# Kernel tuning notes

Hardware: AMD Instinct MI355X
Metric: run time of the kernel (lower is better)

## Reference

```python
import jax, jax.numpy as jnp
import numpy as np

N_USERS, N_ITEMS, EMB_DIM, N_INTENTS, N_EDGES, N_LAYERS = 50000, 100000, 64, 128, 3000000, 2
N_NODES = N_USERS + N_ITEMS


def _l2norm(x, eps=1e-8):
    # F.normalize(p=2, dim=-1, eps): x / max(||x||, eps)
    n = jnp.sqrt(jnp.sum(x * x, axis=-1, keepdims=True))
    return x / jnp.maximum(n, eps)


def setup_inputs() -> dict:
    key = jax.random.key(0)
    k0, k1, k2, k3, k4, k5 = jax.random.split(key, 6)
    xav_e = np.sqrt(2.0 / (N_NODES + EMB_DIM)).astype(np.float32)
    xav_i = np.sqrt(2.0 / (EMB_DIM + N_INTENTS)).astype(np.float32)
    return {
        "user_emb": jax.random.normal(k0, (N_USERS, EMB_DIM), jnp.float32) * xav_e,
        "item_emb": jax.random.normal(k1, (N_ITEMS, EMB_DIM), jnp.float32) * xav_e,
        "user_intent": jax.random.normal(k2, (EMB_DIM, N_INTENTS), jnp.float32) * xav_i,
        "item_intent": jax.random.normal(k3, (EMB_DIM, N_INTENTS), jnp.float32) * xav_i,
        "all_h": jax.random.randint(k4, (N_EDGES,), 0, N_NODES, jnp.int32),
        "all_t": jax.random.randint(k5, (N_EDGES,), 0, N_NODES, jnp.int32),
    }


def reference(user_emb, item_emb, user_intent, item_intent, all_h, all_t):
    E = all_h.shape[0]

    def spmm(vals, x):
        # y[h] += vals * x[t]  over edges  (torch_sparse.spmm)
        return jax.ops.segment_sum(vals[:, None] * x[all_t], all_h, num_segments=N_NODES)

    # _cal_sparse_adj: G = D^-1/2 A D^-1/2 on the unweighted edge list
    deg = jax.ops.segment_sum(jnp.ones((E,), jnp.float32), all_h, num_segments=N_NODES)
    d_inv_sqrt = jnp.where(deg > 0, deg, 1.0) ** -0.5 * (deg > 0)
    g_values = d_inv_sqrt[all_h] * d_inv_sqrt[all_t]

    def adaptive_values(src):
        # _adaptive_mask: cosine-sim edge weights, row-normalized
        he = _l2norm(src[all_h])
        te = _l2norm(src[all_t])
        edge_alpha = (jnp.sum(he * te, axis=1) + 1.0) * 0.5  # in [0,1]
        row_sum = jax.ops.segment_sum(edge_alpha, all_h, num_segments=N_NODES)
        d_inv = jnp.where(row_sum > 0, 1.0 / jnp.where(row_sum > 0, row_sum, 1.0), 0.0)
        return d_inv[all_h] * edge_alpha

    emb = jnp.concatenate([user_emb, item_emb], axis=0)  # [N, d]
    acc = emb
    for _ in range(N_LAYERS):
        gnn = spmm(g_values, emb)
        u, it = emb[:N_USERS], emb[N_USERS:]
        u_int = jax.nn.softmax(u @ user_intent, axis=1) @ user_intent.T
        i_int = jax.nn.softmax(it @ item_intent, axis=1) @ item_intent.T
        int_e = jnp.concatenate([u_int, i_int], axis=0)
        gaa = spmm(adaptive_values(gnn), emb)
        iaa = spmm(adaptive_values(int_e), emb)
        emb = gnn + int_e + gaa + iaa + emb
        acc = acc + emb
    # torch: sum over stacked layer embeddings == initial + each layer output
    return acc
```

## Files before the change

### kernel.cpp

```cpp
#include <hip/hip_runtime.h>
#include <hip/hip_bf16.h>

#define N_USERS   50000
#define N_ITEMS   100000
#define N_NODES   150000
#define DIM       64
#define N_INTENTS 128
#define N_EDGES   3000000
#define PSHIFT    9
#define PROWS     (1 << PSHIFT)
#define NPART     ((N_NODES + PROWS - 1) >> PSHIFT)
#define CHUNK     16384
#define NCHB      ((N_EDGES + CHUNK - 1) / CHUNK)

typedef __attribute__((ext_vector_type(8))) short short8v;
typedef __attribute__((ext_vector_type(4))) float f32x4;

static __device__ __forceinline__ float wsum64(float v){
#pragma unroll
  for (int m = 32; m >= 1; m >>= 1) v += __shfl_xor(v, m, 64);
  return v;
}

template<int CTRL>
static __device__ __forceinline__ float dpp_ror_add(float x){
  int t = __builtin_amdgcn_update_dpp(0, __builtin_bit_cast(int, x),
                                      CTRL, 0xF, 0xF, true);
  return x + __builtin_bit_cast(float, t);
}
static __device__ __forceinline__ float row16_allsum(float x){
  x = dpp_ror_add<0x128>(x);
  x = dpp_ror_add<0x124>(x);
  x = dpp_ror_add<0x122>(x);
  x = dpp_ror_add<0x121>(x);
  return x;
}
template<int CTRL>
static __device__ __forceinline__ float dpp_ror_max(float x){
  int t = __builtin_amdgcn_update_dpp(0, __builtin_bit_cast(int, x),
                                      CTRL, 0xF, 0xF, true);
  return fmaxf(x, __builtin_bit_cast(float, t));
}
static __device__ __forceinline__ float row16_allmax(float x){
  x = dpp_ror_max<0x128>(x);
  x = dpp_ror_max<0x124>(x);
  x = dpp_ror_max<0x122>(x);
  x = dpp_ror_max<0x121>(x);
  return x;
}

static __device__ __forceinline__ unsigned short f2bf(float x){
  __hip_bfloat16 h = __float2bfloat16(x);
  return __builtin_bit_cast(unsigned short, h);
}
static __device__ __forceinline__ float bf_lo(unsigned int v){
  return __builtin_bit_cast(float, v << 16);
}
static __device__ __forceinline__ float bf_hi(unsigned int v){
  return __builtin_bit_cast(float, v & 0xFFFF0000u);
}
static __device__ __forceinline__ float bfval(unsigned short h){
  return __builtin_bit_cast(float, (unsigned int)h << 16);
}
static __device__ __forceinline__ void split2(float x, unsigned short& hi,
                                              unsigned short& lo){
  hi = f2bf(x);
  lo = f2bf(x - bfval(hi));
}

__global__ void k_init(const float* __restrict__ ue, const float* __restrict__ ie,
                       float* __restrict__ emb, float* __restrict__ acc,
                       unsigned short* __restrict__ embb){
  int i = blockIdx.x * 256 + threadIdx.x;
  if (i >= N_NODES * DIM) return;
  float v = (i < N_USERS * DIM) ? ue[i] : ie[i - N_USERS * DIM];
  emb[i] = v; acc[i] = v; embb[i] = f2bf(v);
}

__global__ void k_deg(const int* __restrict__ h, int* __restrict__ deg){
  int e = blockIdx.x * 256 + threadIdx.x;
  if (e < N_EDGES) atomicAdd(&deg[h[e]], 1);
}

__global__ void k_scan1(const int* __restrict__ deg, int* __restrict__ tmp,
                        int* __restrict__ aux){
  __shared__ int s[256];
  int t = threadIdx.x, i = blockIdx.x * 256 + t;
  int v = (i < N_NODES) ? deg[i] : 0;
  s[t] = v; __syncthreads();
  for (int off = 1; off < 256; off <<= 1){
    int x = (t >= off) ? s[t - off] : 0;
    __syncthreads();
    s[t] += x;
    __syncthreads();
  }
  if (i < N_NODES) tmp[i] = s[t];
  if (t == 255) aux[blockIdx.x] = s[255];
}

__global__ __launch_bounds__(1024) void k_scan2(int* __restrict__ aux, int n){
  __shared__ int s[1024];
  int t = threadIdx.x;
  int v = (t < n) ? aux[t] : 0;
  s[t] = v; __syncthreads();
  for (int off = 1; off < 1024; off <<= 1){
    int x = (t >= off) ? s[t - off] : 0;
    __syncthreads();
    s[t] += x;
    __syncthreads();
  }
  if (t < n) aux[t] = s[t] - v;
}

__global__ void k_rowptr(const int* __restrict__ tmp, const int* __restrict__ deg,
                         const int* __restrict__ aux, int* __restrict__ rp,
                         float* __restrict__ dis, int* __restrict__ gcur){
  int i = blockIdx.x * 256 + threadIdx.x;
  if (i < N_NODES){
    int v = aux[i >> 8] + tmp[i] - deg[i];
    rp[i] = v;
    int d = deg[i];
    dis[i] = (d > 0) ? (1.f / sqrtf((float)d)) : 0.f;
    if ((i & (PROWS - 1)) == 0) gcur[i >> PSHIFT] = v;
  }
  if (i == 0) rp[N_NODES] = N_EDGES;
}

__global__ __launch_bounds__(256) void k_part1(const int* __restrict__ h,
                                               const int* __restrict__ t,
                                               int* __restrict__ gcur,
                                               unsigned int* __restrict__ stg){
  __shared__ int hist[NPART];
  __shared__ int base[NPART];
  __shared__ int cnt2[NPART];
  int tid = threadIdx.x;
  int s = blockIdx.x * CHUNK;
  int e = min(s + CHUNK, N_EDGES);
  for (int p = tid; p < NPART; p += 256){ hist[p] = 0; cnt2[p] = 0; }
  __syncthreads();
  for (int i = s + tid; i < e; i += 256)
    atomicAdd(&hist[h[i] >> PSHIFT], 1);
  __syncthreads();
  for (int p = tid; p < NPART; p += 256){
    int c = hist[p];
    base[p] = c ? atomicAdd(&gcur[p], c) : 0;
  }
  __syncthreads();
  for (int i = s + tid; i < e; i += 256){
    int hh = h[i];
    int part = hh >> PSHIFT;
    int pos = base[part] + atomicAdd(&cnt2[part], 1);
    stg[pos] = ((unsigned)t[i] << PSHIFT) | (unsigned)(hh & (PROWS - 1));
  }
}

__global__ __launch_bounds__(256) void k_part2(const int* __restrict__ rp,
                                               const unsigned int* __restrict__ stg,
                                               int* __restrict__ t_csr){
  __shared__ int cur[PROWS];
  int b = blockIdx.x, tid = threadIdx.x;
  int row0 = b << PSHIFT;
  int rows = min(PROWS, N_NODES - row0);
  for (int i = tid; i < rows; i += 256) cur[i] = rp[row0 + i];
  __syncthreads();
  int s = rp[row0], e = rp[row0 + rows];
  for (int i = s + tid; i < e; i += 256){
    unsigned int v = stg[i];
    int pos = atomicAdd(&cur[v & (PROWS - 1)], 1);
    t_csr[pos] = (int)(v >> PSHIFT);
  }
}

__global__ void k_spmm_gnn(const int* __restrict__ rp, const int* __restrict__ t_csr,
                           const float* __restrict__ dis,
                           const unsigned short* __restrict__ embb,
                           float* __restrict__ gnn, unsigned short* __restrict__ hgAB){
  int w = (blockIdx.x * 256 + threadIdx.x) >> 6;
  int lane = threadIdx.x & 63;
  if (w >= N_NODES) return;
  int slot = lane >> 3, sub = lane & 7;
  int s = rp[w], e = rp[w + 1];
  float a0=0.f,a1=0.f,a2=0.f,a3=0.f,a4=0.f,a5=0.f,a6=0.f,a7=0.f;
  for (int i = s + slot; i < e; i += 8){
    int t = t_csr[i];
    float wt = dis[t];
    uint4 ev = *(const uint4*)(embb + (size_t)t * 64 + 8 * sub);
    a0 = fmaf(wt, bf_lo(ev.x), a0); a1 = fmaf(wt, bf_hi(ev.x), a1);
    a2 = fmaf(wt, bf_lo(ev.y), a2); a3 = fmaf(wt, bf_hi(ev.y), a3);
    a4 = fmaf(wt, bf_lo(ev.z), a4); a5 = fmaf(wt, bf_hi(ev.z), a5);
    a6 = fmaf(wt, bf_lo(ev.w), a6); a7 = fmaf(wt, bf_hi(ev.w), a7);
  }
#pragma unroll
  for (int m = 8; m <= 32; m <<= 1){
    a0 += __shfl_xor(a0, m, 64); a1 += __shfl_xor(a1, m, 64);
    a2 += __shfl_xor(a2, m, 64); a3 += __shfl_xor(a3, m, 64);
    a4 += __shfl_xor(a4, m, 64); a5 += __shfl_xor(a5, m, 64);
    a6 += __shfl_xor(a6, m, 64); a7 += __shfl_xor(a7, m, 64);
  }
  float dw = dis[w];
  float g0 = dw*a0, g1 = dw*a1, g2 = dw*a2, g3 = dw*a3;
  float g4 = dw*a4, g5 = dw*a5, g6 = dw*a6, g7 = dw*a7;
  float sq = g0*g0 + g1*g1 + g2*g2 + g3*g3 + g4*g4 + g5*g5 + g6*g6 + g7*g7;
#pragma unroll
  for (int m = 1; m <= 4; m <<= 1) sq += __shfl_xor(sq, m, 64);
  float invn = 1.f / fmaxf(sqrtf(sq), 1e-8f);
  if (slot == 0){
    float4 v0 = make_float4(g0, g1, g2, g3);
    float4 v1 = make_float4(g4, g5, g6, g7);
    ((float4*)gnn)[w * 16 + 2 * sub]     = v0;
    ((float4*)gnn)[w * 16 + 2 * sub + 1] = v1;
    uint4 ob;
    ob.x = (unsigned)f2bf(g0*invn) | ((unsigned)f2bf(g1*invn) << 16);
    ob.y = (unsigned)f2bf(g2*invn) | ((unsigned)f2bf(g3*invn) << 16);
    ob.z = (unsigned)f2bf(g4*invn) | ((unsigned)f2bf(g5*invn) << 16);
    ob.w = (unsigned)f2bf(g6*invn) | ((unsigned)f2bf(g7*invn) << 16);
    *(uint4*)(hgAB + (size_t)w * 128 + 8 * sub) = ob;
  }
}

__global__ void k_wprep(const float* __restrict__ wu, const float* __restrict__ wi,
                        unsigned short* __restrict__ wbuf){
  const float* W = blockIdx.x ? wi : wu;
  unsigned short* seg = wbuf + blockIdx.x * 32768;
  int tid = threadIdx.x;
  for (int i = tid; i < DIM * N_INTENTS; i += 256){
    unsigned short h, l; split2(W[i], h, l);
    seg[16384 + i] = h; seg[24576 + i] = l;
  }
  for (int idx = tid; idx < 16 * 64; idx += 256){
    int f = idx >> 6, lane = idx & 63;
    int nt = f >> 1, ks = f & 1, g = lane >> 4, c = lane & 15;
    int in = 16 * nt + c;
#pragma unroll
    for (int e = 0; e < 8; e++){
      int d = 8 * g + e + 32 * ks;
      unsigned short h, l; split2(W[d * N_INTENTS + in], h, l);
      seg[f * 512 + lane * 8 + e] = h;
      seg[8192 + f * 512 + lane * 8 + e] = l;
    }
  }
}

__global__ __launch_bounds__(256) void k_intent_mfma(
    const unsigned short* __restrict__ wseg, const float* __restrict__ emb,
    unsigned short* __restrict__ out_bf, unsigned short* __restrict__ hgAB,
    int base_node, int count){
  __shared__ __align__(16) unsigned int Pl[4][2048];
  int wid = threadIdx.x >> 6, lane = threadIdx.x & 63;
  int tile = blockIdx.x * 4 + wid;
  if (tile * 16 >= count) return;
  int g = lane >> 4, c = lane & 15;

  const float4* erow = (const float4*)(emb + (size_t)(base_node + tile * 16 + c) * DIM);
  float4 ea0 = erow[2 * g],     eb0 = erow[2 * g + 1];
  float4 ea1 = erow[8 + 2 * g], eb1 = erow[9 + 2 * g];
  short8v ehi[2], elo[2];
  {
    float xs[16] = {ea0.x, ea0.y, ea0.z, ea0.w, eb0.x, eb0.y, eb0.z, eb0.w,
                    ea1.x, ea1.y, ea1.z, ea1.w, eb1.x, eb1.y, eb1.z, eb1.w};
#pragma unroll
    for (int ksi = 0; ksi < 2; ksi++)
#pragma unroll
      for (int e = 0; e < 8; e++){
        unsigned short h, l; split2(xs[ksi * 8 + e], h, l);
        ehi[ksi][e] = (short)h; elo[ksi][e] = (short)l;
      }
  }

  const uint4* w1hi = (const uint4*)wseg;
  const uint4* w1lo = (const uint4*)(wseg + 8192);
  f32x4 acc1[8];
#pragma unroll
  for (int nt = 0; nt < 8; nt++){
    f32x4 a = {0.f, 0.f, 0.f, 0.f};
#pragma unroll
    for (int ks = 0; ks < 2; ks++){
      short8v wh = __builtin_bit_cast(short8v, w1hi[(nt * 2 + ks) * 64 + lane]);
      short8v wl = __builtin_bit_cast(short8v, w1lo[(nt * 2 + ks) * 64 + lane]);
      a = __builtin_amdgcn_mfma_f32_16x16x32_bf16(ehi[ks], wh, a, 0, 0, 0);
      a = __builtin_amdgcn_mfma_f32_16x16x32_bf16(elo[ks], wh, a, 0, 0, 0);
      a = __builtin_amdgcn_mfma_f32_16x16x32_bf16(ehi[ks], wl, a, 0, 0, 0);
    }
    acc1[nt] = a;
  }

  unsigned int* pw = &Pl[wid][0];
#pragma unroll
  for (int r = 0; r < 4; r++){
    float m = acc1[0][r];
#pragma unroll
    for (int nt = 1; nt < 8; nt++) m = fmaxf(m, acc1[nt][r]);
    m = row16_allmax(m);
    float p[8];
    float s = 0.f;
#pragma unroll
    for (int nt = 0; nt < 8; nt++){ p[nt] = __expf(acc1[nt][r] - m); s += p[nt]; }
    s = row16_allsum(s);
    float inv = 1.f / s;
    int node = 4 * g + r;
    int swz = (node & 7) << 2;
    int base = node * 128 + c;
#pragma unroll
    for (int nt = 0; nt < 8; nt++){
      float v = p[nt] * inv;
      unsigned short h, l; split2(v, h, l);
      pw[(base + 16 * nt) ^ swz] = (unsigned int)h | ((unsigned int)l << 16);
    }
  }

  const uint4* pr = (const uint4*)pw;
  short8v phf[4], plf[4];
  int sw = (c & 7) << 2;
#pragma unroll
  for (int ks = 0; ks < 4; ks++){
    int i0 = c * 128 + 8 * g + 32 * ks;
    uint4 ra = pr[(i0 ^ sw) >> 2];
    uint4 rb = pr[((i0 + 4) ^ sw) >> 2];
    unsigned int q[8] = {ra.x, ra.y, ra.z, ra.w, rb.x, rb.y, rb.z, rb.w};
#pragma unroll
    for (int e = 0; e < 8; e++){
      phf[ks][e] = (short)(q[e] & 0xFFFFu);
      plf[ks][e] = (short)(q[e] >> 16);
    }
  }

  const uint4* w2hi = (const uint4*)(wseg + 16384);
  const uint4* w2lo = (const uint4*)(wseg + 24576);
  f32x4 acc2[4];
#pragma unroll
  for (int nt = 0; nt < 4; nt++){
    f32x4 a = {0.f, 0.f, 0.f, 0.f};
#pragma unroll
    for (int ks = 0; ks < 4; ks++){
      int fi = (16 * nt + c) * 16 + ks * 4 + g;
      short8v wh = __builtin_bit_cast(short8v, w2hi[fi]);
      short8v wl = __builtin_bit_cast(short8v, w2lo[fi]);
      a = __builtin_amdgcn_mfma_f32_16x16x32_bf16(phf[ks], wh, a, 0, 0, 0);
      a = __builtin_amdgcn_mfma_f32_16x16x32_bf16(plf[ks], wh, a, 0, 0, 0);
      a = __builtin_amdgcn_mfma_f32_16x16x32_bf16(phf[ks], wl, a, 0, 0, 0);
    }
    acc2[nt] = a;
  }

#pragma unroll
  for (int r = 0; r < 4; r++){
    float sq = 0.f;
#pragma unroll
    for (int nt = 0; nt < 4; nt++) sq = fmaf(acc2[nt][r], acc2[nt][r], sq);
    sq = row16_allsum(sq);
    float invn = 1.f / fmaxf(sqrtf(sq), 1e-8f);
    size_t node = (size_t)(base_node + tile * 16 + 4 * g + r);
    unsigned short* hw = hgAB + node * 128 + 64;
    size_t obase = node * DIM + c;
#pragma unroll
    for (int nt = 0; nt < 4; nt++){
      float v = acc2[nt][r];
      out_bf[obase + 16 * nt] = f2bf(v);
      hw[16 * nt + c] = f2bf(v * invn);
    }
  }
}

__global__ void k_adafuse(const int* __restrict__ rp, const int* __restrict__ t_csr,
                          const uint4* __restrict__ hgAB4,
                          const uint2* __restrict__ inte_bf2,
                          const uint2* __restrict__ embb2,
                          const float* __restrict__ emb,
                          float* __restrict__ gnn_io, float* __restrict__ acc,
                          uint2* __restrict__ embb_next2){
  int w = (blockIdx.x * 256 + threadIdx.x) >> 6;
  int lane = threadIdx.x & 63;
  if (w >= N_NODES) return;
  int slot = lane >> 4, sub = lane & 15;
  uint4 hp = hgAB4[(size_t)w * 16 + sub];
  float w0 = bf_lo(hp.x), w1 = bf_hi(hp.x), w2 = bf_lo(hp.y), w3 = bf_hi(hp.y);
  float w4 = bf_lo(hp.z), w5 = bf_hi(hp.z), w6 = bf_lo(hp.w), w7 = bf_hi(hp.w);
  bool isA = sub < 8;
  int s = rp[w], e = rp[w + 1];
  float4 s1 = make_float4(0.f, 0.f, 0.f, 0.f);
  float4 s2 = make_float4(0.f, 0.f, 0.f, 0.f);
  float r1 = 0.f, r2 = 0.f;
  for (int i = s + slot; i < e; i += 4){
    int t = t_csr[i];
    uint4 tp = hgAB4[(size_t)t * 16 + sub];
    float part = w0 * bf_lo(tp.x) + w1 * bf_hi(tp.x)
               + w2 * bf_lo(tp.y) + w3 * bf_hi(tp.y)
               + w4 * bf_lo(tp.z) + w5 * bf_hi(tp.z)
               + w6 * bf_lo(tp.w) + w7 * bf_hi(tp.w);
    float p = row16_allsum(isA ? part : 0.f);
    float q = row16_allsum(isA ? 0.f : part);
    float a1 = fmaf(p, 0.5f, 0.5f);
    float a2 = fmaf(q, 0.5f, 0.5f);
    r1 += a1; r2 += a2;
    uint2 ev = embb2[(size_t)t * 16 + sub];
    float v0 = bf_lo(ev.x), v1 = bf_hi(ev.x), v2 = bf_lo(ev.y), v3 = bf_hi(ev.y);
    s1.x = fmaf(a1, v0, s1.x); s1.y = fmaf(a1, v1, s1.y);
    s1.z = fmaf(a1, v2, s1.z); s1.w = fmaf(a1, v3, s1.w);
    s2.x = fmaf(a2, v0, s2.x); s2.y = fmaf(a2, v1, s2.y);
    s2.z = fmaf(a2, v2, s2.z); s2.w = fmaf(a2, v3, s2.w);
  }
#pragma unroll
  for (int m = 16; m <= 32; m <<= 1){
    s1.x += __shfl_xor(s1.x, m, 64); s1.y += __shfl_xor(s1.y, m, 64);
    s1.z += __shfl_xor(s1.z, m, 64); s1.w += __shfl_xor(s1.w, m, 64);
    s2.x += __shfl_xor(s2.x, m, 64); s2.y += __shfl_xor(s2.y, m, 64);
    s2.z += __shfl_xor(s2.z, m, 64); s2.w += __shfl_xor(s2.w, m, 64);
    r1   += __shfl_xor(r1,   m, 64); r2   += __shfl_xor(r2,   m, 64);
  }
  float d1 = (r1 > 0.f) ? 1.f / r1 : 0.f;
  float d2 = (r2 > 0.f) ? 1.f / r2 : 0.f;
  if (slot == 0){
    int idx4 = w * 16 + sub;
    float4 gg = ((float4*)gnn_io)[idx4];
    uint2 it = inte_bf2[idx4];
    float4 em = ((const float4*)emb)[idx4];
    float4 nv;
    nv.x = gg.x + bf_lo(it.x) + em.x + d1 * s1.x + d2 * s2.x;
    nv.y = gg.y + bf_hi(it.x) + em.y + d1 * s1.y + d2 * s2.y;
    nv.z = gg.z + bf_lo(it.y) + em.z + d1 * s1.z + d2 * s2.z;
    nv.w = gg.w + bf_hi(it.y) + em.w + d1 * s1.w + d2 * s2.w;
    ((float4*)gnn_io)[idx4] = nv;
    float4 ac = ((float4*)acc)[idx4];
    ac.x += nv.x; ac.y += nv.y; ac.z += nv.z; ac.w += nv.w;
    ((float4*)acc)[idx4] = ac;
    uint2 ob;
    ob.x = (unsigned)f2bf(nv.x) | ((unsigned)f2bf(nv.y) << 16);
    ob.y = (unsigned)f2bf(nv.z) | ((unsigned)f2bf(nv.w) << 16);
    embb_next2[idx4] = ob;
  }
}

extern "C" void kernel_launch(void* const* d_in, const int* in_sizes, int n_in,
                              void* d_out, int out_size, void* d_ws, size_t ws_size,
                              hipStream_t stream){
  const float* ue = (const float*)d_in[0];
  const float* ie = (const float*)d_in[1];
  const float* wu = (const float*)d_in[2];
  const float* wi = (const float*)d_in[3];
  const int* all_h = (const int*)d_in[4];
  const int* all_t = (const int*)d_in[5];
  float* acc = (float*)d_out;

  char* p = (char*)d_ws;
  auto take = [&](size_t bytes)->char*{
    char* r = p; p += (bytes + 255) & ~size_t(255); return r;
  };
  float*  embA  = (float*)take(sizeof(float) * N_NODES * DIM);
  float*  embB  = (float*)take(sizeof(float) * N_NODES * DIM);
  unsigned short* hgAB = (unsigned short*)take(sizeof(short) * N_NODES * 128);
  unsigned short* inte_bf = (unsigned short*)take(sizeof(short) * N_NODES * DIM);
  unsigned short* embbA   = (unsigned short*)take(sizeof(short) * N_NODES * DIM);
  unsigned short* embbB   = (unsigned short*)take(sizeof(short) * N_NODES * DIM);
  unsigned short* wbuf    = (unsigned short*)take(sizeof(short) * 2 * 32768);
  int*    t_csr = (int*)take(sizeof(int) * N_EDGES);
  float*  dis   = (float*)take(sizeof(float) * N_NODES);
  int*    deg   = (int*)take(sizeof(int) * N_NODES);
  int*    tmp   = (int*)take(sizeof(int) * N_NODES);
  int*    aux   = (int*)take(sizeof(int) * 1024);
  int*    rp    = (int*)take(sizeof(int) * (N_NODES + 1));
  int*    gcur  = (int*)take(sizeof(int) * NPART);
  if ((size_t)(p - (char*)d_ws) > ws_size) return;
  unsigned int* stg = (unsigned int*)hgAB;

  const int ELEM_B  = (N_NODES * DIM + 255) / 256;
  const int NODEW_B = (N_NODES * 64 + 255) / 256;
  const int EDGE_B  = (N_EDGES + 255) / 256;
  const int NODE_B  = (N_NODES + 255) / 256;

  hipMemsetAsync(deg, 0, sizeof(int) * N_NODES, stream);
  k_init<<<ELEM_B, 256, 0, stream>>>(ue, ie, embA, acc, embbA);
  k_wprep<<<2, 256, 0, stream>>>(wu, wi, wbuf);
  k_deg<<<EDGE_B, 256, 0, stream>>>(all_h, deg);
  k_scan1<<<NODE_B, 256, 0, stream>>>(deg, tmp, aux);
  k_scan2<<<1, 1024, 0, stream>>>(aux, NODE_B);
  k_rowptr<<<NODE_B, 256, 0, stream>>>(tmp, deg, aux, rp, dis, gcur);
  k_part1<<<NCHB, 256, 0, stream>>>(all_h, all_t, gcur, stg);
  k_part2<<<NPART, 256, 0, stream>>>(rp, stg, t_csr);

  const int UT_B = ((N_USERS / 16) + 3) / 4;
  const int IT_B = ((N_ITEMS / 16) + 3) / 4;

  float* eA = embA;
  float* eB = embB;
  unsigned short* ebA = embbA;
  unsigned short* ebB = embbB;
  for (int layer = 0; layer < 2; layer++){
    k_spmm_gnn<<<NODEW_B, 256, 0, stream>>>(rp, t_csr, dis, ebA, eB, hgAB);
    k_intent_mfma<<<UT_B, 256, 0, stream>>>(wbuf, eA, inte_bf, hgAB, 0, N_USERS);
    k_intent_mfma<<<IT_B, 256, 0, stream>>>(wbuf + 32768, eA, inte_bf, hgAB,
                                            N_USERS, N_ITEMS);
    k_adafuse<<<NODEW_B, 256, 0, stream>>>(rp, t_csr, (const uint4*)hgAB,
                                           (const uint2*)inte_bf,
                                           (const uint2*)ebA,
                                           eA, eB, acc, (uint2*)ebB);
    float* t = eA; eA = eB; eB = t;
    unsigned short* tb = ebA; ebA = ebB; ebB = tb;
  }
}
```

Measured before the change: 1.008 ms.

## Store normalized edge-similarity embeddings in FP8 and pre-scale gathered embeddings by degree

```diff
diff --git a/kernel.cpp b/kernel.cpp
--- a/kernel.cpp
+++ b/kernel.cpp
@@ -15,12 +15,7 @@
 
 typedef __attribute__((ext_vector_type(8))) short short8v;
 typedef __attribute__((ext_vector_type(4))) float f32x4;
-
-static __device__ __forceinline__ float wsum64(float v){
-#pragma unroll
-  for (int m = 32; m >= 1; m >>= 1) v += __shfl_xor(v, m, 64);
-  return v;
-}
+typedef __attribute__((ext_vector_type(2))) float f32x2;
 
 template<int CTRL>
 static __device__ __forceinline__ float dpp_ror_add(float x){
@@ -66,6 +61,18 @@
                                               unsigned short& lo){
   hi = f2bf(x);
   lo = f2bf(x - bfval(hi));
+}
+
+static __device__ __forceinline__ void fp8dec8(uint2 v, float* f){
+  f32x2 a = __builtin_amdgcn_cvt_pk_f32_fp8(v.x, false);
+  f32x2 b = __builtin_amdgcn_cvt_pk_f32_fp8(v.x, true);
+  f32x2 c = __builtin_amdgcn_cvt_pk_f32_fp8(v.y, false);
+  f32x2 d = __builtin_amdgcn_cvt_pk_f32_fp8(v.y, true);
+  f[0]=a[0]; f[1]=a[1]; f[2]=b[0]; f[3]=b[1];
+  f[4]=c[0]; f[5]=c[1]; f[6]=d[0]; f[7]=d[1];
+}
+static __device__ __forceinline__ unsigned char f2fp8(float x){
+  return (unsigned char)(__builtin_amdgcn_cvt_pk_fp8_f32(x, x, 0, false) & 0xFF);
 }
 
 __global__ void k_init(const float* __restrict__ ue, const float* __restrict__ ie,
@@ -75,6 +82,18 @@
   if (i >= N_NODES * DIM) return;
   float v = (i < N_USERS * DIM) ? ue[i] : ie[i - N_USERS * DIM];
   emb[i] = v; acc[i] = v; embb[i] = f2bf(v);
+}
+
+__global__ void k_embd0(const float* __restrict__ emb, const float* __restrict__ dis,
+                        uint2* __restrict__ embd2){
+  int i = blockIdx.x * 256 + threadIdx.x;
+  if (i >= N_NODES * 16) return;
+  float d = dis[i >> 4];
+  float4 v = ((const float4*)emb)[i];
+  uint2 ob;
+  ob.x = (unsigned)f2bf(d * v.x) | ((unsigned)f2bf(d * v.y) << 16);
+  ob.y = (unsigned)f2bf(d * v.z) | ((unsigned)f2bf(d * v.w) << 16);
+  embd2[i] = ob;
 }
 
 __global__ void k_deg(const int* __restrict__ h, int* __restrict__ deg){
@@ -173,8 +192,8 @@
 
 __global__ void k_spmm_gnn(const int* __restrict__ rp, const int* __restrict__ t_csr,
                            const float* __restrict__ dis,
-                           const unsigned short* __restrict__ embb,
-                           float* __restrict__ gnn, unsigned short* __restrict__ hgAB){
+                           const unsigned short* __restrict__ embd,
+                           float* __restrict__ gnn, unsigned char* __restrict__ hg8){
   int w = (blockIdx.x * 256 + threadIdx.x) >> 6;
   int lane = threadIdx.x & 63;
   if (w >= N_NODES) return;
@@ -183,12 +202,11 @@
   float a0=0.f,a1=0.f,a2=0.f,a3=0.f,a4=0.f,a5=0.f,a6=0.f,a7=0.f;
   for (int i = s + slot; i < e; i += 8){
     int t = t_csr[i];
-    float wt = dis[t];
-    uint4 ev = *(const uint4*)(embb + (size_t)t * 64 + 8 * sub);
-    a0 = fmaf(wt, bf_lo(ev.x), a0); a1 = fmaf(wt, bf_hi(ev.x), a1);
-    a2 = fmaf(wt, bf_lo(ev.y), a2); a3 = fmaf(wt, bf_hi(ev.y), a3);
-    a4 = fmaf(wt, bf_lo(ev.z), a4); a5 = fmaf(wt, bf_hi(ev.z), a5);
-    a6 = fmaf(wt, bf_lo(ev.w), a6); a7 = fmaf(wt, bf_hi(ev.w), a7);
+    uint4 ev = *(const uint4*)(embd + (size_t)t * 64 + 8 * sub);
+    a0 += bf_lo(ev.x); a1 += bf_hi(ev.x);
+    a2 += bf_lo(ev.y); a3 += bf_hi(ev.y);
+    a4 += bf_lo(ev.z); a5 += bf_hi(ev.z);
+    a6 += bf_lo(ev.w); a7 += bf_hi(ev.w);
   }
 #pragma unroll
   for (int m = 8; m <= 32; m <<= 1){
@@ -209,12 +227,12 @@
     float4 v1 = make_float4(g4, g5, g6, g7);
     ((float4*)gnn)[w * 16 + 2 * sub]     = v0;
     ((float4*)gnn)[w * 16 + 2 * sub + 1] = v1;
-    uint4 ob;
-    ob.x = (unsigned)f2bf(g0*invn) | ((unsigned)f2bf(g1*invn) << 16);
-    ob.y = (unsigned)f2bf(g2*invn) | ((unsigned)f2bf(g3*invn) << 16);
-    ob.z = (unsigned)f2bf(g4*invn) | ((unsigned)f2bf(g5*invn) << 16);
-    ob.w = (unsigned)f2bf(g6*invn) | ((unsigned)f2bf(g7*invn) << 16);
-    *(uint4*)(hgAB + (size_t)w * 128 + 8 * sub) = ob;
+    unsigned int d0 = __builtin_amdgcn_cvt_pk_fp8_f32(g0*invn, g1*invn, 0, false);
+    d0 = __builtin_amdgcn_cvt_pk_fp8_f32(g2*invn, g3*invn, d0, true);
+    unsigned int d1 = __builtin_amdgcn_cvt_pk_fp8_f32(g4*invn, g5*invn, 0, false);
+    d1 = __builtin_amdgcn_cvt_pk_fp8_f32(g6*invn, g7*invn, d1, true);
+    uint2 o; o.x = d0; o.y = d1;
+    *(uint2*)(hg8 + (size_t)w * 128 + 8 * sub) = o;
   }
 }
 
@@ -243,7 +261,7 @@
 
 __global__ __launch_bounds__(256) void k_intent_mfma(
     const unsigned short* __restrict__ wseg, const float* __restrict__ emb,
-    unsigned short* __restrict__ out_bf, unsigned short* __restrict__ hgAB,
+    unsigned short* __restrict__ out_bf, unsigned char* __restrict__ hg8,
     int base_node, int count){
   __shared__ __align__(16) unsigned int Pl[4][2048];
   int wid = threadIdx.x >> 6, lane = threadIdx.x & 63;
@@ -350,31 +368,33 @@
     sq = row16_allsum(sq);
     float invn = 1.f / fmaxf(sqrtf(sq), 1e-8f);
     size_t node = (size_t)(base_node + tile * 16 + 4 * g + r);
-    unsigned short* hw = hgAB + node * 128 + 64;
+    unsigned char* hw = hg8 + node * 128 + 64;
     size_t obase = node * DIM + c;
 #pragma unroll
     for (int nt = 0; nt < 4; nt++){
       float v = acc2[nt][r];
       out_bf[obase + 16 * nt] = f2bf(v);
-      hw[16 * nt + c] = f2bf(v * invn);
+      hw[16 * nt + c] = f2fp8(v * invn);
     }
   }
 }
 
 __global__ void k_adafuse(const int* __restrict__ rp, const int* __restrict__ t_csr,
-                          const uint4* __restrict__ hgAB4,
+                          const unsigned char* __restrict__ hg8,
                           const uint2* __restrict__ inte_bf2,
                           const uint2* __restrict__ embb2,
                           const float* __restrict__ emb,
+                          const float* __restrict__ dis,
                           float* __restrict__ gnn_io, float* __restrict__ acc,
-                          uint2* __restrict__ embb_next2){
+                          uint2* __restrict__ embb_next2,
+                          uint2* __restrict__ embd_next2){
   int w = (blockIdx.x * 256 + threadIdx.x) >> 6;
   int lane = threadIdx.x & 63;
   if (w >= N_NODES) return;
   int slot = lane >> 4, sub = lane & 15;
-  uint4 hp = hgAB4[(size_t)w * 16 + sub];
-  float w0 = bf_lo(hp.x), w1 = bf_hi(hp.x), w2 = bf_lo(hp.y), w3 = bf_hi(hp.y);
-  float w4 = bf_lo(hp.z), w5 = bf_hi(hp.z), w6 = bf_lo(hp.w), w7 = bf_hi(hp.w);
+  const uint2* hg2 = (const uint2*)hg8;
+  float wv[8];
+  fp8dec8(hg2[(size_t)w * 16 + sub], wv);
   bool isA = sub < 8;
   int s = rp[w], e = rp[w + 1];
   float4 s1 = make_float4(0.f, 0.f, 0.f, 0.f);
@@ -382,13 +402,16 @@
   float r1 = 0.f, r2 = 0.f;
   for (int i = s + slot; i < e; i += 4){
     int t = t_csr[i];
-    uint4 tp = hgAB4[(size_t)t * 16 + sub];
-    float part = w0 * bf_lo(tp.x) + w1 * bf_hi(tp.x)
-               + w2 * bf_lo(tp.y) + w3 * bf_hi(tp.y)
-               + w4 * bf_lo(tp.z) + w5 * bf_hi(tp.z)
-               + w6 * bf_lo(tp.w) + w7 * bf_hi(tp.w);
-    float p = row16_allsum(isA ? part : 0.f);
-    float q = row16_allsum(isA ? 0.f : part);
+    float tv[8];
+    fp8dec8(hg2[(size_t)t * 16 + sub], tv);
+    float part = wv[0]*tv[0] + wv[1]*tv[1] + wv[2]*tv[2] + wv[3]*tv[3]
+               + wv[4]*tv[4] + wv[5]*tv[5] + wv[6]*tv[6] + wv[7]*tv[7];
+    part += __shfl_xor(part, 1, 64);
+    part += __shfl_xor(part, 2, 64);
+    part += __shfl_xor(part, 4, 64);
+    float other = __shfl_xor(part, 8, 64);
+    float p = isA ? part : other;
+    float q = isA ? other : part;
     float a1 = fmaf(p, 0.5f, 0.5f);
     float a2 = fmaf(q, 0.5f, 0.5f);
     r1 += a1; r2 += a2;
@@ -427,6 +450,11 @@
     ob.x = (unsigned)f2bf(nv.x) | ((unsigned)f2bf(nv.y) << 16);
     ob.y = (unsigned)f2bf(nv.z) | ((unsigned)f2bf(nv.w) << 16);
     embb_next2[idx4] = ob;
+    float dw = dis[w];
+    uint2 od;
+    od.x = (unsigned)f2bf(dw * nv.x) | ((unsigned)f2bf(dw * nv.y) << 16);
+    od.y = (unsigned)f2bf(dw * nv.z) | ((unsigned)f2bf(dw * nv.w) << 16);
+    embd_next2[idx4] = od;
   }
 }
 
@@ -447,10 +475,11 @@
   };
   float*  embA  = (float*)take(sizeof(float) * N_NODES * DIM);
   float*  embB  = (float*)take(sizeof(float) * N_NODES * DIM);
-  unsigned short* hgAB = (unsigned short*)take(sizeof(short) * N_NODES * 128);
+  unsigned char* hg8 = (unsigned char*)take((size_t)N_NODES * 128);
   unsigned short* inte_bf = (unsigned short*)take(sizeof(short) * N_NODES * DIM);
   unsigned short* embbA   = (unsigned short*)take(sizeof(short) * N_NODES * DIM);
   unsigned short* embbB   = (unsigned short*)take(sizeof(short) * N_NODES * DIM);
+  unsigned short* embd    = (unsigned short*)take(sizeof(short) * N_NODES * DIM);
   unsigned short* wbuf    = (unsigned short*)take(sizeof(short) * 2 * 32768);
   int*    t_csr = (int*)take(sizeof(int) * N_EDGES);
   float*  dis   = (float*)take(sizeof(float) * N_NODES);
@@ -460,9 +489,10 @@
   int*    rp    = (int*)take(sizeof(int) * (N_NODES + 1));
   int*    gcur  = (int*)take(sizeof(int) * NPART);
   if ((size_t)(p - (char*)d_ws) > ws_size) return;
-  unsigned int* stg = (unsigned int*)hgAB;
+  unsigned int* stg = (unsigned int*)hg8;
 
   const int ELEM_B  = (N_NODES * DIM + 255) / 256;
+  const int ELEM4_B = (N_NODES * 16 + 255) / 256;
   const int NODEW_B = (N_NODES * 64 + 255) / 256;
   const int EDGE_B  = (N_EDGES + 255) / 256;
   const int NODE_B  = (N_NODES + 255) / 256;
@@ -474,6 +504,7 @@
   k_scan1<<<NODE_B, 256, 0, stream>>>(deg, tmp, aux);
   k_scan2<<<1, 1024, 0, stream>>>(aux, NODE_B);
   k_rowptr<<<NODE_B, 256, 0, stream>>>(tmp, deg, aux, rp, dis, gcur);
+  k_embd0<<<ELEM4_B, 256, 0, stream>>>(embA, dis, (uint2*)embd);
   k_part1<<<NCHB, 256, 0, stream>>>(all_h, all_t, gcur, stg);
   k_part2<<<NPART, 256, 0, stream>>>(rp, stg, t_csr);
 
@@ -485,14 +516,15 @@
   unsigned short* ebA = embbA;
   unsigned short* ebB = embbB;
   for (int layer = 0; layer < 2; layer++){
-    k_spmm_gnn<<<NODEW_B, 256, 0, stream>>>(rp, t_csr, dis, ebA, eB, hgAB);
-    k_intent_mfma<<<UT_B, 256, 0, stream>>>(wbuf, eA, inte_bf, hgAB, 0, N_USERS);
-    k_intent_mfma<<<IT_B, 256, 0, stream>>>(wbuf + 32768, eA, inte_bf, hgAB,
+    k_spmm_gnn<<<NODEW_B, 256, 0, stream>>>(rp, t_csr, dis, embd, eB, hg8);
+    k_intent_mfma<<<UT_B, 256, 0, stream>>>(wbuf, eA, inte_bf, hg8, 0, N_USERS);
+    k_intent_mfma<<<IT_B, 256, 0, stream>>>(wbuf + 32768, eA, inte_bf, hg8,
                                             N_USERS, N_ITEMS);
-    k_adafuse<<<NODEW_B, 256, 0, stream>>>(rp, t_csr, (const uint4*)hgAB,
+    k_adafuse<<<NODEW_B, 256, 0, stream>>>(rp, t_csr, hg8,
                                            (const uint2*)inte_bf,
                                            (const uint2*)ebA,
-                                           eA, eB, acc, (uint2*)ebB);
+                                           eA, dis, eB, acc,
+                                           (uint2*)ebB, (uint2*)embd);
     float* t = eA; eA = eB; eB = t;
     unsigned short* tb = ebA; ebA = ebB; ebB = tb;
   }
```

Measured after the change: 948.9 us. 5.9% less time.
